# Performance work log

Measured on AMD Instinct MI355X. Metric: run time of the kernel, lower is better.

## Reference

```python
import jax, jax.numpy as jnp
import numpy as np

B, T, V, C, D = 32, 512, 25, 64, 128
EPS = 1e-5


def _shift_indices(num_nodes, ch, sign):
    i = np.arange(num_nodes)[:, None]
    j = np.arange(ch)[None, :]
    idx = (i * ch + j + sign * j * ch) % (ch * num_nodes)
    return jnp.asarray(idx.reshape(-1).astype(np.int32))


def setup_inputs() -> dict:
    key = jax.random.key(0)
    ks = jax.random.split(key, 6)
    return {
        "x0": jax.random.normal(ks[0], (B, T, V, C), jnp.float32),
        "feature_mask": jax.random.normal(ks[1], (1, V, C), jnp.float32) * 0.1,
        "W": jax.random.normal(ks[2], (C, D), jnp.float32) * (1.0 / np.sqrt(D)),
        "lin_b": jax.random.normal(ks[3], (1, 1, D), jnp.float32) * 0.02,
        "bn_gamma": jnp.ones((V * D,), jnp.float32),
        "bn_beta": jnp.zeros((V * D,), jnp.float32),
        "down_w": jax.random.normal(ks[4], (D, C), jnp.float32) * (1.0 / np.sqrt(C)),
        "down_b": jax.random.normal(ks[5], (D,), jnp.float32) * 0.02,
        "dbn_gamma": jnp.ones((D,), jnp.float32),
        "dbn_beta": jnp.zeros((D,), jnp.float32),
        "shift_in": _shift_indices(V, C, +1),
        "shift_out": _shift_indices(V, D, -1),
    }


def reference(x0, feature_mask, W, lin_b, bn_gamma, bn_beta,
              down_w, down_b, dbn_gamma, dbn_beta, shift_in, shift_out):
    b, t, v, c = x0.shape
    d = W.shape[1]
    n = b * t
    # shift-in gather over flattened (V*C) feature axis
    x = x0.reshape(n, v * c)[:, shift_in].reshape(n, v, c)
    # learned feature mask
    x = x * (jnp.tanh(feature_mask) + 1.0)
    # small per-node linear
    x = jnp.einsum('nvc,cd->nvd', x, W) + lin_b
    # shift-out gather
    x = x.reshape(n, v * d)[:, shift_out]
    # BatchNorm1d (training-mode batch stats, biased variance)
    mu = x.mean(0)
    var = x.var(0)
    x = (x - mu) * (bn_gamma / jnp.sqrt(var + EPS)) + bn_beta
    x = x.reshape(b, t, v, d).transpose(0, 3, 1, 2)  # (B, D, T, V)
    # residual down path: 1x1 conv == per-position matmul, then BN2d
    res = jnp.einsum('btvc,dc->btvd', x0, down_w) + down_b
    rmu = res.mean((0, 1, 2))
    rvar = res.var((0, 1, 2))
    res = (res - rmu) * (dbn_gamma / jnp.sqrt(rvar + EPS)) + dbn_beta
    res = res.transpose(0, 3, 1, 2)  # (B, D, T, V)
    return jax.nn.relu(x + res)
```

## Files before the change

### kernel.cpp

```cpp
#include <hip/hip_runtime.h>

#define VC 1600
#define EPSF 1e-5f

#define WS_MASKJ  0
#define WS_WPACK  1600
#define WS_DWPACK 5696
#define WS_ABY    9792
#define WS_ABR    16192
#define WS_COLSUM 16448
#define WS_QYP    18048
#define QYP_STRIDE 3328
#define WS_ABY2   1721984
#define WS_Y_SH   3456768
#define WS_R_SH   55885568
#define WS_NEED_BYTES 216628736ULL

typedef __attribute__((ext_vector_type(8))) short s16x8;
typedef __attribute__((ext_vector_type(4))) short s16x4;
typedef __attribute__((ext_vector_type(4))) float f32x4;

__device__ __forceinline__ short f2bf(float f) {
  unsigned u = __builtin_bit_cast(unsigned, f);
  u += 0x7fffu + ((u >> 16) & 1u);
  return (short)(u >> 16);
}
__device__ __forceinline__ float bf2f(short s) {
  unsigned u = ((unsigned)(unsigned short)s) << 16;
  return __builtin_bit_cast(float, u);
}

__device__ __forceinline__ void stage_elem(int j, int base, int vstr, float4 xv,
                                           const float* mj, short* s_raw, short* s_xm) {
  int u = j >> 6, c = j & 63;
  s16x4 pk; pk[0]=f2bf(xv.x); pk[1]=f2bf(xv.y); pk[2]=f2bf(xv.z); pk[3]=f2bf(xv.w);
  *(s16x4*)(s_raw + (base + u*vstr)*72 + c) = pk;
  int v0 = (u - c + 75) % 25;
  float xa[4] = {xv.x, xv.y, xv.z, xv.w};
#pragma unroll
  for (int e = 0; e < 4; e++) {
    int ve = v0 - e; if (ve < 0) ve += 25;
    s_xm[(base + ve*vstr)*72 + c + e] = f2bf(xa[e] * mj[e]);
  }
}

__global__ void k_init(const float* __restrict__ fm, const float* __restrict__ W,
                       const float* __restrict__ dw, float* __restrict__ ws) {
  int g = blockIdx.x * 256 + threadIdx.x;
  if (g < VC) {
    int c = g & 63, jv = g >> 6;
    int v = (jv - c + 75) % 25;
    ws[WS_MASKJ + g] = tanhf(fm[v * 64 + c]) + 1.0f;
    ws[WS_COLSUM + g] = 0.0f;
  }
  if (g >= 2048 && g < 3072) {
    int idx = g - 2048;
    int frag = idx >> 6, lane = idx & 63;
    int nt = frag >> 1, k = frag & 1, q = lane >> 4, l = lane & 15;
    s16x8 pk;
#pragma unroll
    for (int j = 0; j < 8; j++) {
      int c = k * 32 + q * 8 + j;
      pk[j] = f2bf(W[c * 128 + nt * 16 + l]);
    }
    ((s16x8*)(ws + WS_WPACK))[idx] = pk;
  }
  if (g >= 3072 && g < 4096) {
    int idx = g - 3072;
    int frag = idx >> 6, lane = idx & 63;
    int nt = frag >> 1, k = frag & 1, q = lane >> 4, l = lane & 15;
    s16x8 pk;
#pragma unroll
    for (int j = 0; j < 8; j++) {
      int c = k * 32 + q * 8 + j;
      pk[j] = f2bf(dw[(nt * 16 + l) * 64 + c]);
    }
    ((s16x8*)(ws + WS_DWPACK))[idx] = pk;
  }
}

__launch_bounds__(256, 2)
__global__ void k_stats(const float* __restrict__ x0, float* __restrict__ ws, int do_store) {
  __shared__ short s_raw[14976];
  __shared__ short s_xm[14976];
  __shared__ float s_qy[3328];
  int tid = threadIdx.x;
  int wave = tid >> 6, lane = tid & 63, quad = lane >> 4, l15 = lane & 15;
  for (int t = tid; t < 3328; t += 256) s_qy[t] = 0.f;
  for (int t = tid; t < 576; t += 256) { s_raw[14400 + t] = 0; s_xm[14400 + t] = 0; }
  const s16x8* wpack = (const s16x8*)(ws + WS_WPACK);
  const s16x8* dwpack = (const s16x8*)(ws + WS_DWPACK);
  short* wsy = (short*)ws + WS_Y_SH;
  short* wsr = (short*)ws + WS_R_SH;

  int nt0 = wave * 2;
  s16x8 bw[2][2], bd[2][2];
#pragma unroll
  for (int a = 0; a < 2; a++) {
    int nt = nt0 + a;
    bw[a][0] = wpack[(nt * 2 + 0) * 64 + lane];
    bw[a][1] = wpack[(nt * 2 + 1) * 64 + lane];
    bd[a][0] = dwpack[(nt * 2 + 0) * 64 + lane];
    bd[a][1] = dwpack[(nt * 2 + 1) * 64 + lane];
  }
  float mj0[4], mj1[4];
  {
    float4 m4 = *(const float4*)(ws + WS_MASKJ + tid * 4);
    mj0[0]=m4.x; mj0[1]=m4.y; mj0[2]=m4.z; mj0[3]=m4.w;
  }
  if (tid < 144) {
    float4 m4 = *(const float4*)(ws + WS_MASKJ + 1024 + tid * 4);
    mj1[0]=m4.x; mj1[1]=m4.y; mj1[2]=m4.z; mj1[3]=m4.w;
  }
  float cs[8] = {0,0,0,0,0,0,0,0};
  float rq0 = 0.f, rq1 = 0.f;

  for (int chunk = 0; chunk < 4; chunk++) {
    int n0 = blockIdx.x * 32 + chunk * 8;
    __syncthreads();
    for (int r = 0; r < 8; r++) {
      const float* rowp = x0 + (size_t)(n0 + r) * VC;
      float4 xv = *(const float4*)(rowp + tid * 4);
      cs[0]+=xv.x; cs[1]+=xv.y; cs[2]+=xv.z; cs[3]+=xv.w;
      stage_elem(tid * 4, r, 8, xv, mj0, s_raw, s_xm);
      if (tid < 144) {
        float4 xw = *(const float4*)(rowp + 1024 + tid * 4);
        cs[4]+=xw.x; cs[5]+=xw.y; cs[6]+=xw.z; cs[7]+=xw.w;
        stage_elem(1024 + tid * 4, r, 8, xw, mj1, s_raw, s_xm);
      }
    }
    __syncthreads();
#pragma unroll 1
    for (int vp = 0; vp < 13; vp++) {
      int rb = vp * 16;
      const short* px = s_xm + (rb + l15) * 72 + quad * 8;
      const short* pr = s_raw + (rb + l15) * 72 + quad * 8;
      s16x8 a0 = *(const s16x8*)px;
      s16x8 a1 = *(const s16x8*)(px + 32);
      s16x8 r0 = *(const s16x8*)pr;
      s16x8 r1 = *(const s16x8*)(pr + 32);
      int vq = vp * 2 + (quad >> 1);
#pragma unroll
      for (int a = 0; a < 2; a++) {
        f32x4 acc = {0.f, 0.f, 0.f, 0.f};
        acc = __builtin_amdgcn_mfma_f32_16x16x32_bf16(a0, bw[a][0], acc, 0, 0, 0);
        acc = __builtin_amdgcn_mfma_f32_16x16x32_bf16(a1, bw[a][1], acc, 0, 0, 0);
        float q = acc[0]*acc[0] + acc[1]*acc[1] + acc[2]*acc[2] + acc[3]*acc[3];
        atomicAdd(&s_qy[vq * 128 + (nt0 + a) * 16 + l15], q);
        f32x4 rc = {0.f, 0.f, 0.f, 0.f};
        rc = __builtin_amdgcn_mfma_f32_16x16x32_bf16(r0, bd[a][0], rc, 0, 0, 0);
        rc = __builtin_amdgcn_mfma_f32_16x16x32_bf16(r1, bd[a][1], rc, 0, 0, 0);
        float t2 = rc[0]*rc[0] + rc[1]*rc[1] + rc[2]*rc[2] + rc[3]*rc[3];
        if (a == 0) rq0 += t2; else rq1 += t2;
      }
      if (do_store) {
        int slot = rb + l15;
        int vv2 = slot >> 3, rr2 = slot & 7;
        size_t bsh = (size_t)((n0 + rr2) * 25 + vv2) * 128 + nt0 * 16 + quad * 4;
#pragma unroll
        for (int aa = 0; aa < 2; aa++) {
          f32x4 tY = {0.f, 0.f, 0.f, 0.f};
          tY = __builtin_amdgcn_mfma_f32_16x16x32_bf16(bw[aa][0], a0, tY, 0, 0, 0);
          tY = __builtin_amdgcn_mfma_f32_16x16x32_bf16(bw[aa][1], a1, tY, 0, 0, 0);
          f32x4 tR = {0.f, 0.f, 0.f, 0.f};
          tR = __builtin_amdgcn_mfma_f32_16x16x32_bf16(bd[aa][0], r0, tR, 0, 0, 0);
          tR = __builtin_amdgcn_mfma_f32_16x16x32_bf16(bd[aa][1], r1, tR, 0, 0, 0);
          if (vv2 < 25) {
            s16x4 ky, kr;
#pragma unroll
            for (int e = 0; e < 4; e++) { ky[e] = f2bf(tY[e]); kr[e] = f2bf(tR[e]); }
            *(s16x4*)(wsy + bsh + aa * 16) = ky;
            *(s16x4*)(wsr + bsh + aa * 16) = kr;
          }
        }
      }
    }
  }
  __syncthreads();
  atomicAdd(&s_qy[3200 + nt0 * 16 + l15], rq0);
  atomicAdd(&s_qy[3200 + (nt0 + 1) * 16 + l15], rq1);
  __syncthreads();
  float* qp = ws + WS_QYP + (size_t)blockIdx.x * QYP_STRIDE;
  for (int t = tid; t < 3328; t += 256) qp[t] = s_qy[t];
#pragma unroll
  for (int e = 0; e < 4; e++) atomicAdd(ws + WS_COLSUM + tid * 4 + e, cs[e]);
  if (tid < 144) {
#pragma unroll
    for (int e = 0; e < 4; e++) atomicAdd(ws + WS_COLSUM + 1024 + tid * 4 + e, cs[4 + e]);
  }
}

__global__ void k_reduce(const float* __restrict__ gamma, const float* __restrict__ beta,
                         const float* __restrict__ dgamma, const float* __restrict__ dbeta,
                         const float* __restrict__ W, const float* __restrict__ dw,
                         float* __restrict__ ws, int do_store) {
  int tid = threadIdx.x;
  if (blockIdx.x == 25) {
    __shared__ float s_cs[64];
    if (tid < 64) {
      float s = 0.f;
#pragma unroll
      for (int v = 0; v < 25; v++) s += ws[WS_COLSUM + v * 64 + tid];
      s_cs[tid] = s;
    }
    __syncthreads();
    int d = tid;
    float q = 0.f;
#pragma unroll 8
    for (int b2 = 0; b2 < 512; b2++) q += ws[WS_QYP + (size_t)b2 * QYP_STRIDE + 3200 + d];
    float m = 0.f;
#pragma unroll 8
    for (int c = 0; c < 64; c++) m += s_cs[c] * dw[d * 64 + c];
    m *= (1.0f / 409600.0f);
    float var = q * (1.0f / 409600.0f) - m * m;
    float a = dgamma[d] * rsqrtf(var + EPSF);
    ((float2*)(ws + WS_ABR))[d] = make_float2(a, dbeta[d] - m * a);
    return;
  }
  __shared__ float s_cm[1600];
  for (int t = tid; t < 1600; t += 128)
    s_cm[t] = ws[WS_COLSUM + t] * ws[WS_MASKJ + t];
  __syncthreads();
  int f = blockIdx.x * 128 + tid;
  int v = f >> 7, d = f & 127;
  float q = 0.f;
#pragma unroll 8
  for (int b2 = 0; b2 < 512; b2++) q += ws[WS_QYP + (size_t)b2 * QYP_STRIDE + f];
  float m = 0.f;
  int p = v * 64;
#pragma unroll 8
  for (int c = 0; c < 64; c++) {
    m += s_cm[p] * W[c * 128 + d];
    p += 65; if (p >= VC) p -= VC;
  }
  m *= (1.0f / 16384.0f);
  float var = q * (1.0f / 16384.0f) - m * m;
  int d25 = d % 25;
  int vo = v + d25; if (vo >= 25) vo -= 25;
  int jg = vo * 128 + d;
  float a = gamma[jg] * rsqrtf(var + EPSF);
  float bb = beta[jg] - m * a;
  ((float2*)(ws + WS_ABY))[f] = make_float2(a, bb);
  if (do_store) ((float2*)(ws + WS_ABY2))[vo * 128 + d] = make_float2(a, bb);
}

__launch_bounds__(256, 3)
__global__ void k_out(const float* __restrict__ ws, float* __restrict__ out) {
  __shared__ short s_y[12800];
  __shared__ short s_r[12800];
  int tid = threadIdx.x;
  int n0 = blockIdx.x * 4;
  const short* wsy = (const short*)ws + WS_Y_SH + (size_t)n0 * 3200;
  const short* wsr = (const short*)ws + WS_R_SH + (size_t)n0 * 3200;
  for (int idx = tid; idx < 1600; idx += 256) {
    int tl = idx / 400;
    int rem = idx - tl * 400;
    int v = rem >> 4, dblk = rem & 15;
    int phys = (((tl * 25 + v) << 4) + (dblk ^ (v & 15))) * 8;
    *(s16x8*)(s_y + phys) = *(const s16x8*)(wsy + idx * 8);
    *(s16x8*)(s_r + phys) = *(const s16x8*)(wsr + idx * 8);
  }
  __syncthreads();
  int b = n0 >> 9, t0 = n0 & 511;
  float* ob = out + (size_t)b * 1638400 + (size_t)t0 * 25;
  const float2* aby2 = (const float2*)(ws + WS_ABY2);
  const float2* abrp = (const float2*)(ws + WS_ABR);
  for (int it = tid; it < 3200; it += 256) {
    int dd = it / 25;
    int qg = it - dd * 25;
    int q0 = qg * 4;
    int d25 = dd % 25;
    float2 ar = abrp[dd];
    int tl = q0 / 25;
    int vo = q0 - tl * 25;
    int sh = dd >> 3, dlo = dd & 7;
    float ov[4];
#pragma unroll
    for (int e = 0; e < 4; e++) {
      int vi = vo - d25; if (vi < 0) vi += 25;
      int ady = (((tl * 25 + vi) << 4) + (sh ^ (vi & 15))) * 8 + dlo;
      int adr = (((tl * 25 + vo) << 4) + (sh ^ (vo & 15))) * 8 + dlo;
      float yv = bf2f(s_y[ady]);
      float rv = bf2f(s_r[adr]);
      float2 ay = aby2[vo * 128 + dd];
      ov[e] = fmaxf(yv * ay.x + ay.y + rv * ar.x + ar.y, 0.0f);
      vo++; if (vo == 25) { vo = 0; tl++; }
    }
    float4 o; o.x = ov[0]; o.y = ov[1]; o.z = ov[2]; o.w = ov[3];
    *(float4*)(ob + (size_t)dd * 12800 + q0) = o;
  }
}

__launch_bounds__(256, 2)
__global__ void k_main(const float* __restrict__ x0, const float* __restrict__ ws,
                       float* __restrict__ out) {
  __shared__ short s_raw[112 * 72];
  __shared__ short s_xm[112 * 72];
  __shared__ short s_ybuf[100 * 129];
  int tid = threadIdx.x;
  int wave = tid >> 6, lane = tid & 63, quad = lane >> 4, l15 = lane & 15;
  int n0 = blockIdx.x * 4;
  for (int t = tid; t < 1600; t += 256) {
    int flat = t * 4;
    int nl = flat / VC;
    int j = flat - nl * VC;
    float4 xv = *(const float4*)(x0 + (size_t)n0 * VC + flat);
    float4 m4 = *(const float4*)(ws + WS_MASKJ + j);
    float mj[4] = {m4.x, m4.y, m4.z, m4.w};
    stage_elem(j, nl * 25, 1, xv, mj, (short*)s_raw, (short*)s_xm);
  }
  __syncthreads();
  const s16x8* wpack = (const s16x8*)(ws + WS_WPACK);
  const float2* aby = (const float2*)(ws + WS_ABY);
  {
    s16x8 b0, b1;
#pragma unroll
    for (int ji = 0; ji < 14; ji++) {
      int job = wave * 14 + ji;
      int nt = job / 7, mt = job - nt * 7;
      if (ji == 0 || ji == 7) {
        b0 = wpack[(nt * 2 + 0) * 64 + lane];
        b1 = wpack[(nt * 2 + 1) * 64 + lane];
      }
      int mbase = mt * 16;
      const short* pa = s_xm + (mbase + l15) * 72 + quad * 8;
      s16x8 a0 = *(const s16x8*)(pa);
      s16x8 a1 = *(const s16x8*)(pa + 32);
      f32x4 acc = {0.f, 0.f, 0.f, 0.f};
      acc = __builtin_amdgcn_mfma_f32_16x16x32_bf16(a0, b0, acc, 0, 0, 0);
      acc = __builtin_amdgcn_mfma_f32_16x16x32_bf16(a1, b1, acc, 0, 0, 0);
      int d = nt * 16 + l15;
      int d25 = d % 25;
#pragma unroll
      for (int i = 0; i < 4; i++) {
        int s = mbase + quad * 4 + i;
        if (s < 100) {
          int r = s / 25;
          int vv = s - r * 25;
          float2 ab = aby[vv * 128 + d];
          float val = acc[i] * ab.x + ab.y;
          int vo = vv + d25; if (vo >= 25) vo -= 25;
          s_ybuf[(r * 25 + vo) * 129 + d] = f2bf(val);
        }
      }
    }
  }
  __syncthreads();
  const s16x8* dwpack = (const s16x8*)(ws + WS_DWPACK);
  const float2* abr = (const float2*)(ws + WS_ABR);
  {
    s16x8 b0, b1; float2 ab = make_float2(0.f, 0.f);
#pragma unroll
    for (int ji = 0; ji < 14; ji++) {
      int job = wave * 14 + ji;
      int nt = job / 7, mt = job - nt * 7;
      if (ji == 0 || ji == 7) {
        b0 = dwpack[(nt * 2 + 0) * 64 + lane];
        b1 = dwpack[(nt * 2 + 1) * 64 + lane];
        ab = abr[nt * 16 + l15];
      }
      int mbase = mt * 16;
      const short* pa = s_raw + (mbase + l15) * 72 + quad * 8;
      s16x8 a0 = *(const s16x8*)(pa);
      s16x8 a1 = *(const s16x8*)(pa + 32);
      f32x4 acc = {0.f, 0.f, 0.f, 0.f};
      acc = __builtin_amdgcn_mfma_f32_16x16x32_bf16(a0, b0, acc, 0, 0, 0);
      acc = __builtin_amdgcn_mfma_f32_16x16x32_bf16(a1, b1, acc, 0, 0, 0);
      int d = nt * 16 + l15;
#pragma unroll
      for (int i = 0; i < 4; i++) {
        int s = mbase + quad * 4 + i;
        if (s < 100) {
          int r = s / 25;
          int vv = s - r * 25;
          int ad = (r * 25 + vv) * 129 + d;
          float val = acc[i] * ab.x + ab.y + bf2f(s_ybuf[ad]);
          val = fmaxf(val, 0.0f);
          s_ybuf[ad] = f2bf(val);
        }
      }
    }
  }
  __syncthreads();
  int b = n0 >> 9, t0 = n0 & 511;
  float* ob = out + (size_t)b * 1638400 + (size_t)t0 * 25;
  for (int it = tid; it < 3200; it += 256) {
    int dd = it / 25;
    int qg = it - dd * 25;
    int q0 = qg * 4;
    float4 o;
    o.x = bf2f(s_ybuf[(q0 + 0) * 129 + dd]);
    o.y = bf2f(s_ybuf[(q0 + 1) * 129 + dd]);
    o.z = bf2f(s_ybuf[(q0 + 2) * 129 + dd]);
    o.w = bf2f(s_ybuf[(q0 + 3) * 129 + dd]);
    *(float4*)(ob + (size_t)dd * 12800 + q0) = o;
  }
}

extern "C" void kernel_launch(void* const* d_in, const int* in_sizes, int n_in,
                              void* d_out, int out_size, void* d_ws, size_t ws_size,
                              hipStream_t stream) {
  const float* x0    = (const float*)d_in[0];
  const float* fm    = (const float*)d_in[1];
  const float* W     = (const float*)d_in[2];
  const float* bn_g  = (const float*)d_in[4];
  const float* bn_b  = (const float*)d_in[5];
  const float* dw    = (const float*)d_in[6];
  const float* dbn_g = (const float*)d_in[8];
  const float* dbn_b = (const float*)d_in[9];
  float* ws = (float*)d_ws;
  float* out = (float*)d_out;
  int big = (ws_size >= WS_NEED_BYTES) ? 1 : 0;
  k_init<<<20, 256, 0, stream>>>(fm, W, dw, ws);
  k_stats<<<512, 256, 0, stream>>>(x0, ws, big);
  k_reduce<<<26, 128, 0, stream>>>(bn_g, bn_b, dbn_g, dbn_b, W, dw, ws, big);
  if (big) k_out<<<4096, 256, 0, stream>>>(ws, out);
  else     k_main<<<4096, 256, 0, stream>>>(x0, ws, out);
}
```

Baseline: 624.2 us.

## Shrink stats/output tiles and replace shared-memory atomics with register accumulation

k_stats now stages 4 rows per chunk instead of 8, which halves its LDS footprint. It drops the shared s_qy array and its atomics in favour of per-lane register accumulators, which are written straight to the per-block partials, with shuffle reductions for the residual stats. Its launch bound rises to 4 blocks per CU. k_out handles 2 rows per block with float2 stores and twice as many blocks, to raise occupancy. The trade-off is more register pressure in k_stats and narrower, less coalesced global stores in k_out.

Result: slower. 742.1 us (+18.9%).

```diff
diff --git a/kernel.cpp b/kernel.cpp
--- a/kernel.cpp
+++ b/kernel.cpp
@@ -79,15 +79,13 @@
   }
 }
 
-__launch_bounds__(256, 2)
+__launch_bounds__(256, 4)
 __global__ void k_stats(const float* __restrict__ x0, float* __restrict__ ws, int do_store) {
-  __shared__ short s_raw[14976];
-  __shared__ short s_xm[14976];
-  __shared__ float s_qy[3328];
+  __shared__ short s_raw[8064];
+  __shared__ short s_xm[8064];
   int tid = threadIdx.x;
   int wave = tid >> 6, lane = tid & 63, quad = lane >> 4, l15 = lane & 15;
-  for (int t = tid; t < 3328; t += 256) s_qy[t] = 0.f;
-  for (int t = tid; t < 576; t += 256) { s_raw[14400 + t] = 0; s_xm[14400 + t] = 0; }
+  for (int t = tid; t < 864; t += 256) { s_raw[7200 + t] = 0; s_xm[7200 + t] = 0; }
   const s16x8* wpack = (const s16x8*)(ws + WS_WPACK);
   const s16x8* dwpack = (const s16x8*)(ws + WS_DWPACK);
   short* wsy = (short*)ws + WS_Y_SH;
@@ -114,24 +112,27 @@
   }
   float cs[8] = {0,0,0,0,0,0,0,0};
   float rq0 = 0.f, rq1 = 0.f;
-
-  for (int chunk = 0; chunk < 4; chunk++) {
-    int n0 = blockIdx.x * 32 + chunk * 8;
+  float qy[7][2];
+#pragma unroll
+  for (int i = 0; i < 7; i++) { qy[i][0] = 0.f; qy[i][1] = 0.f; }
+
+  for (int chunk = 0; chunk < 8; chunk++) {
+    int n0 = blockIdx.x * 32 + chunk * 4;
     __syncthreads();
-    for (int r = 0; r < 8; r++) {
+    for (int r = 0; r < 4; r++) {
       const float* rowp = x0 + (size_t)(n0 + r) * VC;
       float4 xv = *(const float4*)(rowp + tid * 4);
       cs[0]+=xv.x; cs[1]+=xv.y; cs[2]+=xv.z; cs[3]+=xv.w;
-      stage_elem(tid * 4, r, 8, xv, mj0, s_raw, s_xm);
+      stage_elem(tid * 4, r, 4, xv, mj0, s_raw, s_xm);
       if (tid < 144) {
         float4 xw = *(const float4*)(rowp + 1024 + tid * 4);
         cs[4]+=xw.x; cs[5]+=xw.y; cs[6]+=xw.z; cs[7]+=xw.w;
-        stage_elem(1024 + tid * 4, r, 8, xw, mj1, s_raw, s_xm);
+        stage_elem(1024 + tid * 4, r, 4, xw, mj1, s_raw, s_xm);
       }
     }
     __syncthreads();
-#pragma unroll 1
-    for (int vp = 0; vp < 13; vp++) {
+#pragma unroll
+    for (int vp = 0; vp < 7; vp++) {
       int rb = vp * 16;
       const short* px = s_xm + (rb + l15) * 72 + quad * 8;
       const short* pr = s_raw + (rb + l15) * 72 + quad * 8;
@@ -139,14 +140,12 @@
       s16x8 a1 = *(const s16x8*)(px + 32);
       s16x8 r0 = *(const s16x8*)pr;
       s16x8 r1 = *(const s16x8*)(pr + 32);
-      int vq = vp * 2 + (quad >> 1);
 #pragma unroll
       for (int a = 0; a < 2; a++) {
         f32x4 acc = {0.f, 0.f, 0.f, 0.f};
         acc = __builtin_amdgcn_mfma_f32_16x16x32_bf16(a0, bw[a][0], acc, 0, 0, 0);
         acc = __builtin_amdgcn_mfma_f32_16x16x32_bf16(a1, bw[a][1], acc, 0, 0, 0);
-        float q = acc[0]*acc[0] + acc[1]*acc[1] + acc[2]*acc[2] + acc[3]*acc[3];
-        atomicAdd(&s_qy[vq * 128 + (nt0 + a) * 16 + l15], q);
+        qy[vp][a] += acc[0]*acc[0] + acc[1]*acc[1] + acc[2]*acc[2] + acc[3]*acc[3];
         f32x4 rc = {0.f, 0.f, 0.f, 0.f};
         rc = __builtin_amdgcn_mfma_f32_16x16x32_bf16(r0, bd[a][0], rc, 0, 0, 0);
         rc = __builtin_amdgcn_mfma_f32_16x16x32_bf16(r1, bd[a][1], rc, 0, 0, 0);
@@ -155,7 +154,7 @@
       }
       if (do_store) {
         int slot = rb + l15;
-        int vv2 = slot >> 3, rr2 = slot & 7;
+        int vv2 = slot >> 2, rr2 = slot & 3;
         size_t bsh = (size_t)((n0 + rr2) * 25 + vv2) * 128 + nt0 * 16 + quad * 4;
 #pragma unroll
         for (int aa = 0; aa < 2; aa++) {
@@ -176,12 +175,21 @@
       }
     }
   }
-  __syncthreads();
-  atomicAdd(&s_qy[3200 + nt0 * 16 + l15], rq0);
-  atomicAdd(&s_qy[3200 + (nt0 + 1) * 16 + l15], rq1);
-  __syncthreads();
   float* qp = ws + WS_QYP + (size_t)blockIdx.x * QYP_STRIDE;
-  for (int t = tid; t < 3328; t += 256) qp[t] = s_qy[t];
+  rq0 += __shfl_xor(rq0, 16); rq0 += __shfl_xor(rq0, 32);
+  rq1 += __shfl_xor(rq1, 16); rq1 += __shfl_xor(rq1, 32);
+  if (quad == 0) {
+    qp[3200 + nt0 * 16 + l15] = rq0;
+    qp[3200 + (nt0 + 1) * 16 + l15] = rq1;
+  }
+#pragma unroll
+  for (int vp = 0; vp < 7; vp++) {
+    int vq = vp * 4 + quad;
+    if (vq < 25) {
+      qp[vq * 128 + nt0 * 16 + l15] = qy[vp][0];
+      qp[vq * 128 + (nt0 + 1) * 16 + l15] = qy[vp][1];
+    }
+  }
 #pragma unroll
   for (int e = 0; e < 4; e++) atomicAdd(ws + WS_COLSUM + tid * 4 + e, cs[e]);
   if (tid < 144) {
@@ -244,15 +252,15 @@
   if (do_store) ((float2*)(ws + WS_ABY2))[vo * 128 + d] = make_float2(a, bb);
 }
 
-__launch_bounds__(256, 3)
+__launch_bounds__(256, 6)
 __global__ void k_out(const float* __restrict__ ws, float* __restrict__ out) {
-  __shared__ short s_y[12800];
-  __shared__ short s_r[12800];
+  __shared__ short s_y[6400];
+  __shared__ short s_r[6400];
   int tid = threadIdx.x;
-  int n0 = blockIdx.x * 4;
+  int n0 = blockIdx.x * 2;
   const short* wsy = (const short*)ws + WS_Y_SH + (size_t)n0 * 3200;
   const short* wsr = (const short*)ws + WS_R_SH + (size_t)n0 * 3200;
-  for (int idx = tid; idx < 1600; idx += 256) {
+  for (int idx = tid; idx < 800; idx += 256) {
     int tl = idx / 400;
     int rem = idx - tl * 400;
     int v = rem >> 4, dblk = rem & 15;
@@ -265,18 +273,18 @@
   float* ob = out + (size_t)b * 1638400 + (size_t)t0 * 25;
   const float2* aby2 = (const float2*)(ws + WS_ABY2);
   const float2* abrp = (const float2*)(ws + WS_ABR);
-  for (int it = tid; it < 3200; it += 256) {
-    int dd = it / 25;
-    int qg = it - dd * 25;
-    int q0 = qg * 4;
+  for (int u = tid; u < 3200; u += 256) {
+    int dd = u / 25;
+    int rem = u - dd * 25;
+    int q0 = rem * 2;
     int d25 = dd % 25;
     float2 ar = abrp[dd];
-    int tl = q0 / 25;
+    int tl = (q0 >= 25) ? 1 : 0;
     int vo = q0 - tl * 25;
     int sh = dd >> 3, dlo = dd & 7;
-    float ov[4];
-#pragma unroll
-    for (int e = 0; e < 4; e++) {
+    float ov[2];
+#pragma unroll
+    for (int e = 0; e < 2; e++) {
       int vi = vo - d25; if (vi < 0) vi += 25;
       int ady = (((tl * 25 + vi) << 4) + (sh ^ (vi & 15))) * 8 + dlo;
       int adr = (((tl * 25 + vo) << 4) + (sh ^ (vo & 15))) * 8 + dlo;
@@ -286,8 +294,8 @@
       ov[e] = fmaxf(yv * ay.x + ay.y + rv * ar.x + ar.y, 0.0f);
       vo++; if (vo == 25) { vo = 0; tl++; }
     }
-    float4 o; o.x = ov[0]; o.y = ov[1]; o.z = ov[2]; o.w = ov[3];
-    *(float4*)(ob + (size_t)dd * 12800 + q0) = o;
+    float2 o; o.x = ov[0]; o.y = ov[1];
+    *(float2*)(ob + (size_t)dd * 12800 + q0) = o;
   }
 }
 
@@ -414,6 +422,6 @@
   k_init<<<20, 256, 0, stream>>>(fm, W, dw, ws);
   k_stats<<<512, 256, 0, stream>>>(x0, ws, big);
   k_reduce<<<26, 128, 0, stream>>>(bn_g, bn_b, dbn_g, dbn_b, W, dw, ws, big);
-  if (big) k_out<<<4096, 256, 0, stream>>>(ws, out);
+  if (big) k_out<<<8192, 256, 0, stream>>>(ws, out);
   else     k_main<<<4096, 256, 0, stream>>>(x0, ws, out);
 }
```
